# Optimization experiments

Hardware: AMD Instinct MI355X
Metric: run time of the kernel (lower is better)

## Reference

```python
import jax, jax.numpy as jnp
import numpy as np

N, D, K = 100000, 128, 15
LN_EPS = 1e-5

def setup_inputs() -> dict:
    key = jax.random.key(0)
    k1, k2, k3, k4, k5 = jax.random.split(key, 5)
    node_features = jax.random.normal(k1, (N, D), dtype=jnp.float32)
    neighbor_idx = jax.random.randint(k2, (N, K), 0, N, dtype=jnp.int32)
    neighbor_counts = jax.random.randint(k3, (N,), 0, K + 1, dtype=jnp.int32)
    W = jax.random.normal(k4, (D, D), dtype=jnp.float32) / np.sqrt(D)
    b = jax.random.normal(k5, (D,), dtype=jnp.float32) * 0.01
    ln_w = jnp.ones((D,), dtype=jnp.float32)
    ln_b = jnp.zeros((D,), dtype=jnp.float32)
    return {"node_features": node_features, "neighbor_idx": neighbor_idx,
            "neighbor_counts": neighbor_counts, "W": W, "b": b,
            "ln_w": ln_w, "ln_b": ln_b}

def reference(node_features, neighbor_idx, neighbor_counts, W, b, ln_w, ln_b):
    Kn = neighbor_idx.shape[1]
    # validity mask over padded neighbor slots: [N, K]
    mask = (jnp.arange(Kn)[None, :] < neighbor_counts[:, None]).astype(node_features.dtype)
    feats = node_features[neighbor_idx]              # [N, K, D] gather
    cnt = jnp.maximum(neighbor_counts, 1).astype(node_features.dtype)
    agg = jnp.einsum('nkd,nk->nd', feats, mask) / cnt[:, None]  # mean over valid
    transformed = agg @ W.T + b                       # nn.Linear
    combined = node_features + transformed            # residual
    mu = jnp.mean(combined, axis=-1, keepdims=True)
    var = jnp.mean(jnp.square(combined - mu), axis=-1, keepdims=True)
    normed = (combined - mu) * jax.lax.rsqrt(var + LN_EPS) * ln_w + ln_b
    updated = jax.nn.relu(normed)
    has_nbrs = (neighbor_counts > 0)[:, None]
    return jnp.where(has_nbrs, updated, node_features)
```

## Files before the change

kernel.cpp:

```cpp
#include <hip/hip_runtime.h>
#include <stdint.h>

#define NN 100000
#define DF 128
#define KN 15
#define LN_EPS 1e-5f

typedef __attribute__((ext_vector_type(8))) short bf16x8;
typedef __attribute__((ext_vector_type(4))) float f32x4;

static __device__ __forceinline__ unsigned short f2bf(float f) {
    union { float f; uint32_t u; } v; v.f = f;
    uint32_t r = v.u + 0x7FFFu + ((v.u >> 16) & 1u);
    return (unsigned short)(r >> 16);
}

__global__ __launch_bounds__(512, 4)
void nagg_kernel(const float* __restrict__ nf,
                 const int* __restrict__ nbr,
                 const int* __restrict__ cnts,
                 const float* __restrict__ W,
                 const float* __restrict__ bias,
                 const float* __restrict__ lnw,
                 const float* __restrict__ lnb,
                 float* __restrict__ out)
{
    __shared__ __align__(16) unsigned char WbS[32768];
    __shared__ __align__(16) unsigned char AtS[32768];
    __shared__ int idxS[128 * 16];
    __shared__ int cntS[128];

    const int tid  = threadIdx.x;
    const int lane = tid & 63;
    const int w    = tid >> 6;
    const int base = blockIdx.x * 128;

    {
        const float4* W4 = (const float4*)W;
        #pragma unroll
        for (int it = 0; it < 8; ++it) {
            int e = it * 2048 + tid * 4;
            float4 v = W4[e >> 2];
            int n = e >> 7;
            int k = e & 127;
            ushort4 h;
            h.x = f2bf(v.x); h.y = f2bf(v.y); h.z = f2bf(v.z); h.w = f2bf(v.w);
            *(ushort4*)(WbS + ((n * 256 + k * 2) ^ ((n & 7) << 4))) = h;
        }
    }

    {
        if (lane < 16) {
            int m = w * 16 + lane;
            int node = base + m;
            cntS[m] = (node < NN) ? cnts[node] : 0;
        }
        #pragma unroll
        for (int it = 0; it < 4; ++it) {
            int e = it * 64 + lane;
            if (e < 240) {
                int mm = e / 15, kk = e - mm * 15;
                int m = w * 16 + mm;
                int node = base + m;
                idxS[m * 16 + kk] = (node < NN) ? nbr[(size_t)node * KN + kk] : 0;
            }
        }
    }

    {
        const int g = lane >> 4;
        const int s = lane & 15;
        #pragma unroll 2
        for (int t = 0; t < 16; ++t) {
            int m = w * 16 + t;
            int cnt = cntS[m];
            float acc[8] = {0.f,0.f,0.f,0.f,0.f,0.f,0.f,0.f};
            #pragma unroll
            for (int st = 0; st < 4; ++st) {
                int k = st * 4 + g;
                int idx = idxS[m * 16 + (k & 15)];
                if (k < cnt) {
                    const float4* p = (const float4*)(nf + (size_t)idx * DF + s * 8);
                    float4 u0 = p[0];
                    float4 u1 = p[1];
                    acc[0]+=u0.x; acc[1]+=u0.y; acc[2]+=u0.z; acc[3]+=u0.w;
                    acc[4]+=u1.x; acc[5]+=u1.y; acc[6]+=u1.z; acc[7]+=u1.w;
                }
            }
            #pragma unroll
            for (int j = 0; j < 8; ++j) {
                acc[j] += __shfl_xor(acc[j], 16);
                acc[j] += __shfl_xor(acc[j], 32);
            }
            if (g == 0) {
                float inv = 1.0f / (float)(cnt > 0 ? cnt : 1);
                uint4 pk;
                pk.x = (uint)f2bf(acc[0]*inv) | ((uint)f2bf(acc[1]*inv) << 16);
                pk.y = (uint)f2bf(acc[2]*inv) | ((uint)f2bf(acc[3]*inv) << 16);
                pk.z = (uint)f2bf(acc[4]*inv) | ((uint)f2bf(acc[5]*inv) << 16);
                pk.w = (uint)f2bf(acc[6]*inv) | ((uint)f2bf(acc[7]*inv) << 16);
                *(uint4*)(AtS + ((m * 256 + s * 16) ^ ((m & 7) << 4))) = pk;
            }
        }
    }

    __syncthreads();

    const int l15 = lane & 15;
    const int q   = lane >> 4;

    bf16x8 afr[4];
    #pragma unroll
    for (int kk = 0; kk < 4; ++kk) {
        int m = w * 16 + l15;
        afr[kk] = *(const bf16x8*)(AtS + ((m * 256 + kk * 64 + q * 16) ^ ((m & 7) << 4)));
    }

    f32x4 acc[8];
    #pragma unroll
    for (int nb = 0; nb < 8; ++nb) acc[nb] = (f32x4){0.f,0.f,0.f,0.f};

    #pragma unroll
    for (int nb = 0; nb < 8; ++nb) {
        #pragma unroll
        for (int kk = 0; kk < 4; ++kk) {
            int n = nb * 16 + l15;
            bf16x8 bfr = *(const bf16x8*)(WbS + ((n * 256 + kk * 64 + q * 16) ^ ((n & 7) << 4)));
            acc[nb] = __builtin_amdgcn_mfma_f32_16x16x32_bf16(afr[kk], bfr, acc[nb], 0, 0, 0);
        }
    }

    float bv[8], lwv[8], lbv[8];
    #pragma unroll
    for (int nb = 0; nb < 8; ++nb) {
        int c = nb * 16 + l15;
        bv[nb]  = bias[c];
        lwv[nb] = lnw[c];
        lbv[nb] = lnb[c];
    }

    #pragma unroll
    for (int r = 0; r < 4; ++r) {
        int mloc = q * 4 + r;
        int m = w * 16 + mloc;
        int node = base + m;
        if (node < NN) {
            int cnt = cntS[m];
            float vals[8], nfv[8];
            float s = 0.f, sq = 0.f;
            #pragma unroll
            for (int nb = 0; nb < 8; ++nb) {
                int c = nb * 16 + l15;
                float nv = nf[(size_t)node * DF + c];
                float comb = nv + acc[nb][r] + bv[nb];
                nfv[nb]  = nv;
                vals[nb] = comb;
                s  += comb;
                sq += comb * comb;
            }
            #pragma unroll
            for (int off = 1; off < 16; off <<= 1) {
                s  += __shfl_xor(s,  off);
                sq += __shfl_xor(sq, off);
            }
            float mu   = s  * (1.0f / 128.0f);
            float var  = sq * (1.0f / 128.0f) - mu * mu;
            float rstd = rsqrtf(var + LN_EPS);
            #pragma unroll
            for (int nb = 0; nb < 8; ++nb) {
                int c = nb * 16 + l15;
                float nrm = (vals[nb] - mu) * rstd * lwv[nb] + lbv[nb];
                float rel = fmaxf(nrm, 0.0f);
                out[(size_t)node * DF + c] = (cnt > 0) ? rel : nfv[nb];
            }
        }
    }
}

extern "C" void kernel_launch(void* const* d_in, const int* in_sizes, int n_in,
                              void* d_out, int out_size, void* d_ws, size_t ws_size,
                              hipStream_t stream) {
    const float* nf   = (const float*)d_in[0];
    const int*   nbr  = (const int*)d_in[1];
    const int*   cnts = (const int*)d_in[2];
    const float* W    = (const float*)d_in[3];
    const float* b    = (const float*)d_in[4];
    const float* lnw  = (const float*)d_in[5];
    const float* lnb  = (const float*)d_in[6];
    float* out = (float*)d_out;

    int blocks = (NN + 127) / 128;
    nagg_kernel<<<blocks, 512, 0, stream>>>(nf, nbr, cnts, W, b, lnw, lnb, out);
}
```

Baseline: 173.5 us.

## Gather neighbor features from a precomputed bf16 copy of node features

Adds a pre-pass kernel that converts the whole node feature table to bf16 in the workspace, then the aggregation kernel gathers neighbors from that half-size table instead of fp32. This halves the bytes moved by the random gather, which is the dominant memory traffic. In exchange it adds a full read of the fp32 table plus a write of the bf16 table, and rounds neighbor values to bf16 before summation rather than after. It falls back to the fp32 path if the workspace is too small.

```diff
diff --git a/kernel.cpp b/kernel.cpp
--- a/kernel.cpp
+++ b/kernel.cpp
@@ -14,9 +14,27 @@
     uint32_t r = v.u + 0x7FFFu + ((v.u >> 16) & 1u);
     return (unsigned short)(r >> 16);
 }
-
+static __device__ __forceinline__ float uasf(uint32_t u) {
+    union { uint32_t u; float f; } v; v.u = u; return v.f;
+}
+
+__global__ __launch_bounds__(256)
+void tobf16_kernel(const float* __restrict__ nf, uint4* __restrict__ tbl) {
+    int i = blockIdx.x * 256 + threadIdx.x;
+    const float4* p = (const float4*)nf + (size_t)i * 2;
+    float4 a = p[0], b = p[1];
+    uint4 pk;
+    pk.x = (uint)f2bf(a.x) | ((uint)f2bf(a.y) << 16);
+    pk.y = (uint)f2bf(a.z) | ((uint)f2bf(a.w) << 16);
+    pk.z = (uint)f2bf(b.x) | ((uint)f2bf(b.y) << 16);
+    pk.w = (uint)f2bf(b.z) | ((uint)f2bf(b.w) << 16);
+    tbl[i] = pk;
+}
+
+template<int TBL>
 __global__ __launch_bounds__(512, 4)
 void nagg_kernel(const float* __restrict__ nf,
+                 const uint4* __restrict__ tbl,
                  const int* __restrict__ nbr,
                  const int* __restrict__ cnts,
                  const float* __restrict__ W,
@@ -80,11 +98,19 @@
                 int k = st * 4 + g;
                 int idx = idxS[m * 16 + (k & 15)];
                 if (k < cnt) {
-                    const float4* p = (const float4*)(nf + (size_t)idx * DF + s * 8);
-                    float4 u0 = p[0];
-                    float4 u1 = p[1];
-                    acc[0]+=u0.x; acc[1]+=u0.y; acc[2]+=u0.z; acc[3]+=u0.w;
-                    acc[4]+=u1.x; acc[5]+=u1.y; acc[6]+=u1.z; acc[7]+=u1.w;
+                    if (TBL) {
+                        uint4 r = tbl[(size_t)idx * 16 + s];
+                        acc[0] += uasf(r.x << 16); acc[1] += uasf(r.x & 0xffff0000u);
+                        acc[2] += uasf(r.y << 16); acc[3] += uasf(r.y & 0xffff0000u);
+                        acc[4] += uasf(r.z << 16); acc[5] += uasf(r.z & 0xffff0000u);
+                        acc[6] += uasf(r.w << 16); acc[7] += uasf(r.w & 0xffff0000u);
+                    } else {
+                        const float4* p = (const float4*)(nf + (size_t)idx * DF + s * 8);
+                        float4 u0 = p[0];
+                        float4 u1 = p[1];
+                        acc[0]+=u0.x; acc[1]+=u0.y; acc[2]+=u0.z; acc[3]+=u0.w;
+                        acc[4]+=u1.x; acc[5]+=u1.y; acc[6]+=u1.z; acc[7]+=u1.w;
+                    }
                 }
             }
             #pragma unroll
@@ -190,5 +216,13 @@
     float* out = (float*)d_out;
 
     int blocks = (NN + 127) / 128;
-    nagg_kernel<<<blocks, 512, 0, stream>>>(nf, nbr, cnts, W, b, lnw, lnb, out);
-}
+    size_t need = (size_t)NN * DF * 2;
+
+    if (ws_size >= need) {
+        uint4* tbl = (uint4*)d_ws;
+        tobf16_kernel<<<(NN * DF / 8 + 255) / 256, 256, 0, stream>>>(nf, tbl);
+        nagg_kernel<1><<<blocks, 512, 0, stream>>>(nf, tbl, nbr, cnts, W, b, lnw, lnb, out);
+    } else {
+        nagg_kernel<0><<<blocks, 512, 0, stream>>>(nf, nullptr, nbr, cnts, W, b, lnw, lnb, out);
+    }
+}
```

Result: no change. 175.8 us (+1.3%).

## Split into bf16 table conversion, gather, and GEMM+LayerNorm kernels

Applied to the files above, without the earlier changes.

Adds a three-kernel path used when workspace is large enough. The first kernel converts node features and W to bf16 once, the second gathers and averages bf16 neighbor rows into a bf16 aggregate buffer, and the third runs the MFMA GEMM with residual, LayerNorm and ReLU. The aim is to halve the bytes moved by the random-access neighbor gather, which dominates traffic. In exchange it adds extra full passes to write and read the bf16 table and the aggregate, two more kernel launches, and bf16 rounding of the inputs before summation.

```diff
diff --git a/kernel.cpp b/kernel.cpp
--- a/kernel.cpp
+++ b/kernel.cpp
@@ -14,16 +14,147 @@
     uint32_t r = v.u + 0x7FFFu + ((v.u >> 16) & 1u);
     return (unsigned short)(r >> 16);
 }
+static __device__ __forceinline__ float uasf(uint32_t u) {
+    union { uint32_t u; float f; } v; v.u = u; return v.f;
+}
+static __device__ __forceinline__ uint4 pack8(const float* a) {
+    uint4 pk;
+    pk.x = (uint)f2bf(a[0]) | ((uint)f2bf(a[1]) << 16);
+    pk.y = (uint)f2bf(a[2]) | ((uint)f2bf(a[3]) << 16);
+    pk.z = (uint)f2bf(a[4]) | ((uint)f2bf(a[5]) << 16);
+    pk.w = (uint)f2bf(a[6]) | ((uint)f2bf(a[7]) << 16);
+    return pk;
+}
+
+template<int DOW>
+__global__ __launch_bounds__(256)
+void conv_kernel(const float* __restrict__ nf, const float* __restrict__ W,
+                 uint4* __restrict__ tbl, uint4* __restrict__ wb)
+{
+    int b = blockIdx.x;
+    const float* src; uint4* dst; int i;
+    if (DOW && b >= 6250) { i = (b - 6250) * 256 + threadIdx.x; src = W; dst = wb; }
+    else                  { i = b * 256 + threadIdx.x;          src = nf; dst = tbl; }
+    const float4* p = (const float4*)src + (size_t)i * 2;
+    float4 a = p[0], c = p[1];
+    float v[8] = {a.x, a.y, a.z, a.w, c.x, c.y, c.z, c.w};
+    dst[i] = pack8(v);
+}
+
+__global__ __launch_bounds__(256, 6)
+void gather_kernel(const uint4* __restrict__ tbl, const int* __restrict__ nbr,
+                   const int* __restrict__ cnts, uint4* __restrict__ agg)
+{
+    const int tid  = threadIdx.x;
+    const int s    = tid & 15;
+    const int node = blockIdx.x * 16 + (tid >> 4);
+    const int cnt  = cnts[node];
+    int idxreg = (s < KN) ? nbr[(size_t)node * KN + s] : 0;
+
+    float acc[8] = {0.f,0.f,0.f,0.f,0.f,0.f,0.f,0.f};
+    #pragma unroll
+    for (int st = 0; st < KN; ++st) {
+        int idx = __shfl(idxreg, st, 16);
+        if (st < cnt) {
+            uint4 r = tbl[(size_t)idx * 16 + s];
+            acc[0] += uasf(r.x << 16); acc[1] += uasf(r.x & 0xffff0000u);
+            acc[2] += uasf(r.y << 16); acc[3] += uasf(r.y & 0xffff0000u);
+            acc[4] += uasf(r.z << 16); acc[5] += uasf(r.z & 0xffff0000u);
+            acc[6] += uasf(r.w << 16); acc[7] += uasf(r.w & 0xffff0000u);
+        }
+    }
+    float inv = 1.0f / (float)(cnt > 0 ? cnt : 1);
+    float v[8];
+    #pragma unroll
+    for (int j = 0; j < 8; ++j) v[j] = acc[j] * inv;
+    agg[(size_t)node * 16 + s] = pack8(v);
+}
+
+__global__ __launch_bounds__(256, 4)
+void gemm_kernel(const uint4* __restrict__ agg, const uint4* __restrict__ wb,
+                 const float* __restrict__ nf, const int* __restrict__ cnts,
+                 const float* __restrict__ bias, const float* __restrict__ lnw,
+                 const float* __restrict__ lnb, float* __restrict__ out)
+{
+    const int tid  = threadIdx.x;
+    const int lane = tid & 63;
+    const int w    = tid >> 6;
+    const int l15  = lane & 15;
+    const int q    = lane >> 4;
+    const int base = blockIdx.x * 64;
+
+    int mrow = base + w * 16 + l15;
+    if (mrow >= NN) mrow = NN - 1;
+
+    bf16x8 afr[4];
+    #pragma unroll
+    for (int kk = 0; kk < 4; ++kk)
+        afr[kk] = ((const bf16x8*)agg)[(size_t)mrow * 16 + kk * 4 + q];
+
+    f32x4 acc[8];
+    #pragma unroll
+    for (int nb = 0; nb < 8; ++nb) acc[nb] = (f32x4){0.f,0.f,0.f,0.f};
+
+    #pragma unroll
+    for (int nb = 0; nb < 8; ++nb) {
+        int n = nb * 16 + l15;
+        #pragma unroll
+        for (int kk = 0; kk < 4; ++kk) {
+            bf16x8 bfr = ((const bf16x8*)wb)[n * 16 + kk * 4 + q];
+            acc[nb] = __builtin_amdgcn_mfma_f32_16x16x32_bf16(afr[kk], bfr, acc[nb], 0, 0, 0);
+        }
+    }
+
+    float bv[8], lwv[8], lbv[8];
+    #pragma unroll
+    for (int nb = 0; nb < 8; ++nb) {
+        int c = nb * 16 + l15;
+        bv[nb]  = bias[c];
+        lwv[nb] = lnw[c];
+        lbv[nb] = lnb[c];
+    }
+
+    #pragma unroll
+    for (int r = 0; r < 4; ++r) {
+        int node = base + w * 16 + q * 4 + r;
+        if (node < NN) {
+            int cnt = cnts[node];
+            float vals[8], nfv[8];
+            float s = 0.f, sq = 0.f;
+            #pragma unroll
+            for (int nb = 0; nb < 8; ++nb) {
+                int c = nb * 16 + l15;
+                float nv = nf[(size_t)node * DF + c];
+                float comb = nv + acc[nb][r] + bv[nb];
+                nfv[nb]  = nv;
+                vals[nb] = comb;
+                s  += comb;
+                sq += comb * comb;
+            }
+            #pragma unroll
+            for (int off = 1; off < 16; off <<= 1) {
+                s  += __shfl_xor(s,  off);
+                sq += __shfl_xor(sq, off);
+            }
+            float mu   = s  * (1.0f / 128.0f);
+            float var  = sq * (1.0f / 128.0f) - mu * mu;
+            float rstd = rsqrtf(var + LN_EPS);
+            #pragma unroll
+            for (int nb = 0; nb < 8; ++nb) {
+                int c = nb * 16 + l15;
+                float nrm = (vals[nb] - mu) * rstd * lwv[nb] + lbv[nb];
+                float rel = fmaxf(nrm, 0.0f);
+                out[(size_t)node * DF + c] = (cnt > 0) ? rel : nfv[nb];
+            }
+        }
+    }
+}
 
 __global__ __launch_bounds__(512, 4)
-void nagg_kernel(const float* __restrict__ nf,
-                 const int* __restrict__ nbr,
-                 const int* __restrict__ cnts,
-                 const float* __restrict__ W,
-                 const float* __restrict__ bias,
-                 const float* __restrict__ lnw,
-                 const float* __restrict__ lnb,
-                 float* __restrict__ out)
+void fused_kernel(const float* __restrict__ nf, const int* __restrict__ nbr,
+                  const int* __restrict__ cnts, const float* __restrict__ W,
+                  const float* __restrict__ bias, const float* __restrict__ lnw,
+                  const float* __restrict__ lnb, float* __restrict__ out)
 {
     __shared__ __align__(16) unsigned char WbS[32768];
     __shared__ __align__(16) unsigned char AtS[32768];
@@ -41,14 +172,12 @@
         for (int it = 0; it < 8; ++it) {
             int e = it * 2048 + tid * 4;
             float4 v = W4[e >> 2];
-            int n = e >> 7;
-            int k = e & 127;
+            int n = e >> 7, k = e & 127;
             ushort4 h;
             h.x = f2bf(v.x); h.y = f2bf(v.y); h.z = f2bf(v.z); h.w = f2bf(v.w);
             *(ushort4*)(WbS + ((n * 256 + k * 2) ^ ((n & 7) << 4))) = h;
         }
     }
-
     {
         if (lane < 16) {
             int m = w * 16 + lane;
@@ -66,7 +195,6 @@
             }
         }
     }
-
     {
         const int g = lane >> 4;
         const int s = lane & 15;
@@ -94,32 +222,26 @@
             }
             if (g == 0) {
                 float inv = 1.0f / (float)(cnt > 0 ? cnt : 1);
-                uint4 pk;
-                pk.x = (uint)f2bf(acc[0]*inv) | ((uint)f2bf(acc[1]*inv) << 16);
-                pk.y = (uint)f2bf(acc[2]*inv) | ((uint)f2bf(acc[3]*inv) << 16);
-                pk.z = (uint)f2bf(acc[4]*inv) | ((uint)f2bf(acc[5]*inv) << 16);
-                pk.w = (uint)f2bf(acc[6]*inv) | ((uint)f2bf(acc[7]*inv) << 16);
-                *(uint4*)(AtS + ((m * 256 + s * 16) ^ ((m & 7) << 4))) = pk;
-            }
-        }
-    }
-
+                float v[8];
+                #pragma unroll
+                for (int j = 0; j < 8; ++j) v[j] = acc[j] * inv;
+                *(uint4*)(AtS + ((m * 256 + s * 16) ^ ((m & 7) << 4))) = pack8(v);
+            }
+        }
+    }
     __syncthreads();
 
     const int l15 = lane & 15;
     const int q   = lane >> 4;
-
     bf16x8 afr[4];
     #pragma unroll
     for (int kk = 0; kk < 4; ++kk) {
         int m = w * 16 + l15;
         afr[kk] = *(const bf16x8*)(AtS + ((m * 256 + kk * 64 + q * 16) ^ ((m & 7) << 4)));
     }
-
     f32x4 acc[8];
     #pragma unroll
     for (int nb = 0; nb < 8; ++nb) acc[nb] = (f32x4){0.f,0.f,0.f,0.f};
-
     #pragma unroll
     for (int nb = 0; nb < 8; ++nb) {
         #pragma unroll
@@ -129,7 +251,6 @@
             acc[nb] = __builtin_amdgcn_mfma_f32_16x16x32_bf16(afr[kk], bfr, acc[nb], 0, 0, 0);
         }
     }
-
     float bv[8], lwv[8], lbv[8];
     #pragma unroll
     for (int nb = 0; nb < 8; ++nb) {
@@ -138,11 +259,9 @@
         lwv[nb] = lnw[c];
         lbv[nb] = lnb[c];
     }
-
     #pragma unroll
     for (int r = 0; r < 4; ++r) {
-        int mloc = q * 4 + r;
-        int m = w * 16 + mloc;
+        int m = w * 16 + q * 4 + r;
         int node = base + m;
         if (node < NN) {
             int cnt = cntS[m];
@@ -189,6 +308,18 @@
     const float* lnb  = (const float*)d_in[6];
     float* out = (float*)d_out;
 
-    int blocks = (NN + 127) / 128;
-    nagg_kernel<<<blocks, 512, 0, stream>>>(nf, nbr, cnts, W, b, lnw, lnb, out);
-}
+    const size_t tblB = (size_t)NN * 256;
+    const size_t aggB = (size_t)NN * 256;
+    const size_t wbB  = 32768;
+
+    if (ws_size >= tblB + aggB + wbB) {
+        uint4* tbl = (uint4*)d_ws;
+        uint4* agg = (uint4*)((char*)d_ws + tblB);
+        uint4* wb  = (uint4*)((char*)d_ws + tblB + aggB);
+        conv_kernel<1><<<6258, 256, 0, stream>>>(nf, W, tbl, wb);
+        gather_kernel<<<NN / 16, 256, 0, stream>>>(tbl, nbr, cnts, agg);
+        gemm_kernel<<<(NN + 63) / 64, 256, 0, stream>>>(agg, wb, nf, cnts, b, lnw, lnb, out);
+    } else {
+        fused_kernel<<<(NN + 127) / 128, 512, 0, stream>>>(nf, nbr, cnts, W, b, lnw, lnb, out);
+    }
+}
```

Result: slower. 178.7 us (+3.0%).
